# Optimization experiments

Hardware: AMD Instinct MI355X
Metric: run time of the kernel (lower is better)

The kernel has to match this reference:

```python
import jax, jax.numpy as jnp
import numpy as np

N_NODES = 50000
N_EDGES = 800000
IN_FEATS = 32
OUT_FEATS = 32
NUM_HEADS = 4


def setup_inputs() -> dict:
    key = jax.random.key(0)
    ks = jax.random.split(key, 12)
    H, F, IN = NUM_HEADS, OUT_FEATS, IN_FEATS
    h = jax.random.normal(ks[0], (N_NODES, IN), dtype=jnp.float32)
    src = jax.random.randint(ks[1], (N_EDGES,), 0, N_NODES, dtype=jnp.int64)
    dst = jax.random.randint(ks[2], (N_EDGES,), 0, N_NODES, dtype=jnp.int64)
    s = 0.1
    W_gat = jax.random.normal(ks[3], (IN, H * F), dtype=jnp.float32) * s
    attn_l = jax.random.normal(ks[4], (H, F), dtype=jnp.float32) * s
    attn_r = jax.random.normal(ks[5], (H, F), dtype=jnp.float32) * s
    W_ih = jax.random.normal(ks[6], (3 * F, H * F), dtype=jnp.float32) * s
    W_hh = jax.random.normal(ks[7], (3 * F, F), dtype=jnp.float32) * s
    b_ih = jax.random.normal(ks[8], (3 * F,), dtype=jnp.float32) * s
    b_hh = jax.random.normal(ks[9], (3 * F,), dtype=jnp.float32) * s
    return {"h": h, "W_gat": W_gat, "attn_l": attn_l, "attn_r": attn_r,
            "W_ih": W_ih, "W_hh": W_hh, "b_ih": b_ih, "b_hh": b_hh,
            "src": src, "dst": dst}


def reference(h, W_gat, attn_l, attn_r, W_ih, W_hh, b_ih, b_hh, src, dst):
    N = h.shape[0]
    H, F = attn_l.shape
    # --- GATConv ---
    feat = (h @ W_gat).reshape(N, H, F)                      # (N,H,F)
    el = jnp.einsum('nhf,hf->nh', feat, attn_l)              # (N,H)
    er = jnp.einsum('nhf,hf->nh', feat, attn_r)              # (N,H)
    e = jax.nn.leaky_relu(el[src] + er[dst], 0.2)            # (E,H) edge logits
    emax = jax.ops.segment_max(e, dst, num_segments=N)       # per-dst max (stable)
    ee = jnp.exp(e - emax[dst])
    denom = jax.ops.segment_sum(ee, dst, num_segments=N)
    alpha = ee / denom[dst]                                  # segment softmax (E,H)
    msg = feat[src] * alpha[:, :, None]                      # (E,H,F)
    agg = jax.ops.segment_sum(msg, dst, num_segments=N)      # (N,H,F)
    x = agg.reshape(N, H * F)
    # --- GRUCell (torch semantics, gate order r,z,n) ---
    gi = x @ W_ih.T + b_ih                                   # (N,3F)
    gh = h @ W_hh.T + b_hh                                   # (N,3F)
    i_r, i_z, i_n = jnp.split(gi, 3, axis=1)
    h_r, h_z, h_n = jnp.split(gh, 3, axis=1)
    r = jax.nn.sigmoid(i_r + h_r)
    z = jax.nn.sigmoid(i_z + h_z)
    n = jnp.tanh(i_n + r * h_n)
    h_new = (1.0 - z) * n + z * h
    return jax.nn.elu(h_new)
```

## Files before the change

### kernel.cpp

```cpp
#include <hip/hip_runtime.h>
#include <hip/hip_bf16.h>
#include <cmath>

#define N_NODES 50000
#define N_EDGES 800000
#define CAP 64

#define NBINS 196
#define BIN_CAP 8192
#define CUR_PAD 32

#define WCB_ITEMS (144 * 32)
#define WCB_BLOCKS (WCB_ITEMS / 256)
#define WC_ITEMS (192 * 160)
#define WC_BLOCKS (WC_ITEMS / 256)

#define P1_EPT 8
#define P1_EPB (256 * P1_EPT)
#define P1_BLOCKS ((N_EDGES + P1_EPB - 1) / P1_EPB)
#define FEAT_BLOCKS ((N_NODES / 16 + 3) / 4)

typedef __attribute__((ext_vector_type(8))) short bf16x8;
typedef __attribute__((ext_vector_type(4))) float f32x4;

__device__ inline short bfbits(float x) {
    __hip_bfloat16 t = __float2bfloat16(x);
    return *reinterpret_cast<short*>(&t);
}

__device__ inline unsigned char f32_to_fp8(float x) {
    return (unsigned char)(__builtin_amdgcn_cvt_pk_fp8_f32(x, x, 0, false) & 0xff);
}

__global__ __launch_bounds__(256) void k_prep0(
        const float* __restrict__ Wg, const float* __restrict__ al,
        const float* __restrict__ ar, const float* __restrict__ Wih,
        const float* __restrict__ Whh, __hip_bfloat16* __restrict__ Wcomb,
        __hip_bfloat16* __restrict__ Wc, int* __restrict__ bin_cursor) {
    const int t = threadIdx.x;
    if (blockIdx.x < WCB_BLOCKS) {
        const int idx = blockIdx.x * 256 + t;
        const int row = idx >> 5, k = idx & 31;
        float v = 0.f;
        if (row < 128) {
            v = Wg[k * 128 + row];
        } else if (row < 136) {
            const int hd = (row - 128) & 3;
            const float* a = (row < 132) ? (al + hd * 32) : (ar + hd * 32);
            const float* w = Wg + k * 128 + hd * 32;
#pragma unroll
            for (int f = 0; f < 32; ++f) v = fmaf(w[f], a[f], v);
        }
        Wcomb[idx] = __float2bfloat16(v);
        return;
    }
    if (blockIdx.x < WCB_BLOCKS + WC_BLOCKS) {
        const int idx = (blockIdx.x - WCB_BLOCKS) * 256 + t;
        const int r = idx / 160, k = idx - r * 160;
        float v = 0.f;
        if (r < 96) { if (k < 128) v = Wih[r * 128 + k]; }
        else        { if (k >= 128) v = Whh[(r - 96) * 32 + (k - 128)]; }
        Wc[idx] = __float2bfloat16(v);
        return;
    }
    if (t < NBINS) bin_cursor[t * CUR_PAD] = 0;
}

__global__ __launch_bounds__(256) void k_part_feat(
        const float* __restrict__ h, const __hip_bfloat16* __restrict__ Wcomb,
        const int* __restrict__ src, const int* __restrict__ dst,
        int* __restrict__ bin_cursor, unsigned* __restrict__ bin_buf,
        unsigned char* __restrict__ feat, float* __restrict__ el,
        float* __restrict__ er) {
    const int t = threadIdx.x;
    if (blockIdx.x < P1_BLOCKS) {
        __shared__ int bcnt[256], bofs[256], cur[256], gbase[256];
        __shared__ int wt4[4];
        __shared__ unsigned stage[P1_EPB];
        bcnt[t] = 0;
        __syncthreads();
        int bn[P1_EPT];
        unsigned pk[P1_EPT];
        const int ebase = blockIdx.x * P1_EPB + t * P1_EPT;
        if (ebase < N_EDGES) {
            int dd[P1_EPT], ss[P1_EPT];
            *(int4*)(dd)     = *(const int4*)(dst + ebase);
            *(int4*)(dd + 4) = *(const int4*)(dst + ebase + 4);
            *(int4*)(ss)     = *(const int4*)(src + ebase);
            *(int4*)(ss + 4) = *(const int4*)(src + ebase + 4);
#pragma unroll
            for (int q = 0; q < P1_EPT; ++q) {
                bn[q] = dd[q] >> 8;
                pk[q] = (unsigned)ss[q] | ((unsigned)(dd[q] & 255) << 16);
                atomicAdd(&bcnt[bn[q]], 1);
            }
        } else {
#pragma unroll
            for (int q = 0; q < P1_EPT; ++q) bn[q] = -1;
        }
        __syncthreads();
        {
            const int wave = t >> 6, lane = t & 63;
            const int vv = bcnt[t];
            int x = vv;
#pragma unroll
            for (int m = 1; m < 64; m <<= 1) {
                const int y = __shfl_up(x, m, 64);
                if (lane >= m) x += y;
            }
            if (lane == 63) wt4[wave] = x;
            __syncthreads();
            int wb = 0;
#pragma unroll
            for (int i = 0; i < 4; ++i) if (i < wave) wb += wt4[i];
            const int off = wb + x - vv;
            bofs[t] = off;
            cur[t] = off;
            gbase[t] = (vv > 0) ? atomicAdd(&bin_cursor[t * CUR_PAD], vv) : 0;
        }
        __syncthreads();
#pragma unroll
        for (int q = 0; q < P1_EPT; ++q)
            if (bn[q] >= 0) stage[atomicAdd(&cur[bn[q]], 1)] = pk[q];
        __syncthreads();
        if (t < NBINS) {
            const int c = bcnt[t], o = bofs[t], g = gbase[t];
            unsigned* bb = bin_buf + (size_t)t * BIN_CAP;
            for (int j = 0; j < c; ++j) {
                const int gi = g + j;
                if (gi < BIN_CAP) bb[gi] = stage[o + j];
            }
        }
        return;
    }
    __shared__ unsigned char sbuf8[4][16][136];
    const int lane = t & 63, wave = t >> 6;
    const int li = lane & 15, quad = lane >> 4;
    const int mt = (blockIdx.x - P1_BLOCKS) * 4 + wave;
    if (mt >= N_NODES / 16) return;
    const int m_base = mt * 16;
    bf16x8 a;
    {
        const float4* hp = (const float4*)(h + (size_t)(m_base + li) * 32 + quad * 8);
        const float4 f0 = hp[0], f1 = hp[1];
        a[0] = bfbits(f0.x); a[1] = bfbits(f0.y); a[2] = bfbits(f0.z); a[3] = bfbits(f0.w);
        a[4] = bfbits(f1.x); a[5] = bfbits(f1.y); a[6] = bfbits(f1.z); a[7] = bfbits(f1.w);
    }
    f32x4 acc[9];
#pragma unroll
    for (int j = 0; j < 9; ++j) acc[j] = (f32x4){0.f, 0.f, 0.f, 0.f};
#pragma unroll
    for (int j = 0; j < 9; ++j) {
        const bf16x8 b = *(const bf16x8*)(Wcomb + (size_t)(j * 16 + li) * 32 + quad * 8);
        acc[j] = __builtin_amdgcn_mfma_f32_16x16x32_bf16(a, b, acc[j], 0, 0, 0);
    }
#pragma unroll
    for (int j = 0; j < 8; ++j)
#pragma unroll
        for (int i = 0; i < 4; ++i)
            sbuf8[wave][quad * 4 + i][j * 16 + li] = f32_to_fp8(acc[j][i]);
    __builtin_amdgcn_wave_barrier();
#pragma unroll
    for (int rep = 0; rep < 4; ++rep) {
        const int row = rep * 4 + quad;
        const unsigned long long v = *(const unsigned long long*)(&sbuf8[wave][row][li * 8]);
        *(unsigned long long*)(feat + (size_t)(m_base + row) * 128 + li * 8) = v;
    }
    if (li < 8) {
#pragma unroll
        for (int i = 0; i < 4; ++i) {
            const int m = m_base + quad * 4 + i;
            if (li < 4) el[m * 4 + li] = acc[8][i];
            else        er[m * 4 + (li - 4)] = acc[8][i];
        }
    }
}

__global__ __launch_bounds__(256) void k_scat2(
        const int* __restrict__ bin_cursor, const unsigned* __restrict__ bin_buf,
        int* __restrict__ srcs_p, int* __restrict__ counts) {
    __shared__ int lcnt[256];
    const int t = threadIdx.x;
    const int b = blockIdx.x;
    lcnt[t] = 0;
    __syncthreads();
    const int cb = min(bin_cursor[b * CUR_PAD], BIN_CAP);
    const uint4* bb4 = (const uint4*)(bin_buf + (size_t)b * BIN_CAP);
    for (int i = t * 4; i < cb; i += 1024) {
        const uint4 p4 = bb4[i >> 2];
#pragma unroll
        for (int k = 0; k < 4; ++k) {
            if (i + k < cb) {
                const unsigned p = (&p4.x)[k];
                const int dl = p >> 16;
                const int s = p & 0xffff;
                const int pos = atomicAdd(&lcnt[dl], 1);
                if (pos < CAP) srcs_p[(size_t)(b * 256 + dl) * CAP + pos] = s;
            }
        }
    }
    __syncthreads();
    const int node = b * 256 + t;
    if (node < N_NODES) counts[node] = lcnt[t];
}

__global__ __launch_bounds__(256) void k_aggr_gru(
        const int* __restrict__ counts, const int* __restrict__ srcs_p,
        const unsigned char* __restrict__ feat,
        const float* __restrict__ el, const float* __restrict__ er,
        const float* __restrict__ h, const __hip_bfloat16* __restrict__ Wc,
        const float* __restrict__ bih, const float* __restrict__ bhh,
        float* __restrict__ out) {
    __shared__ __hip_bfloat16 xh_tile[16][160];
    __shared__ int   sl_s[4][4][64];
    __shared__ float ex[2][3][16][16];
    const int wave = threadIdx.x >> 6;
    const int lane = threadIdx.x & 63;
    const int eh = lane >> 5;
    const int fl = lane & 31;
    const int hq = fl >> 3;
    const int mbase = blockIdx.x * 16;

    int cnts[4];
#pragma unroll
    for (int u = 0; u < 4; ++u) {
        const int n = mbase + wave * 4 + u;
        cnts[u] = min(counts[n], CAP);
        if (lane < cnts[u]) sl_s[wave][u][lane] = srcs_p[(size_t)n * CAP + lane];
    }
    __builtin_amdgcn_wave_barrier();
    for (int u = 0; u < 4; ++u) {
        const int row = wave * 4 + u;
        const int n = mbase + row;
        const int cnt = cnts[u];
        const int* sl = sl_s[wave][u];
        const float ern = er[n * 4 + hq];
        float a0 = 0.f, a1 = 0.f, a2 = 0.f, a3 = 0.f, psum = 0.f;
        for (int i = 0; i < cnt; i += 16) {
            int  s[8];
            unsigned uq[8];
            float w[8];
#pragma unroll
            for (int j = 0; j < 8; ++j) {
                const int e2 = i + 2 * j + eh;
                s[j] = (e2 < cnt) ? sl[e2] : 0;
            }
#pragma unroll
            for (int j = 0; j < 8; ++j)
                uq[j] = *(const unsigned*)(feat + (size_t)s[j] * 128 + fl * 4);
#pragma unroll
            for (int j = 0; j < 8; ++j)
                w[j] = el[s[j] * 4 + hq];
#pragma unroll
            for (int j = 0; j < 8; ++j) {
                float v = w[j] + ern;
                v = v > 0.f ? v : 0.2f * v;
                w[j] = (i + 2 * j + eh < cnt) ? __expf(v) : 0.f;
                psum += w[j];
            }
#pragma unroll
            for (int j = 0; j < 8; ++j) {
                a0 = fmaf(w[j], __builtin_amdgcn_cvt_f32_fp8(uq[j], 0), a0);
                a1 = fmaf(w[j], __builtin_amdgcn_cvt_f32_fp8(uq[j], 1), a1);
                a2 = fmaf(w[j], __builtin_amdgcn_cvt_f32_fp8(uq[j], 2), a2);
                a3 = fmaf(w[j], __builtin_amdgcn_cvt_f32_fp8(uq[j], 3), a3);
            }
        }
        a0 += __shfl_xor(a0, 32, 64);
        a1 += __shfl_xor(a1, 32, 64);
        a2 += __shfl_xor(a2, 32, 64);
        a3 += __shfl_xor(a3, 32, 64);
        psum += __shfl_xor(psum, 1, 64);
        psum += __shfl_xor(psum, 2, 64);
        psum += __shfl_xor(psum, 4, 64);
        psum += __shfl_xor(psum, 32, 64);
        const float inv = (cnt > 0) ? 8.f / psum : 0.f;
        if (lane < 32) {
            __hip_bfloat162 p0, p1;
            p0.x = __float2bfloat16(a0 * inv); p0.y = __float2bfloat16(a1 * inv);
            p1.x = __float2bfloat16(a2 * inv); p1.y = __float2bfloat16(a3 * inv);
            __hip_bfloat162* xp = (__hip_bfloat162*)&xh_tile[row][0];
            xp[lane * 2]     = p0;
            xp[lane * 2 + 1] = p1;
            xh_tile[row][128 + lane] = __float2bfloat16(h[(size_t)n * 32 + lane]);
        }
    }
    __syncthreads();

    const int li = lane & 15, quad = lane >> 4;
    const int cb = wave >> 1;
    const int ghrole = wave & 1;
    bf16x8 a[5];
#pragma unroll
    for (int s = 0; s < 5; ++s)
        a[s] = *(const bf16x8*)((const char*)&xh_tile[0][0] + li * 320 + s * 64 + quad * 16);
    f32x4 acc[3];
#pragma unroll
    for (int g = 0; g < 3; ++g) {
        acc[g] = (f32x4){0.f, 0.f, 0.f, 0.f};
        const int j = g * 2 + cb + ghrole * 6;
        const bf16x8* bp = (const bf16x8*)(Wc + (size_t)(j * 16 + li) * 160 + quad * 8);
        acc[g] = __builtin_amdgcn_mfma_f32_16x16x32_bf16(a[0], bp[0],  acc[g], 0, 0, 0);
        acc[g] = __builtin_amdgcn_mfma_f32_16x16x32_bf16(a[1], bp[4],  acc[g], 0, 0, 0);
        acc[g] = __builtin_amdgcn_mfma_f32_16x16x32_bf16(a[2], bp[8],  acc[g], 0, 0, 0);
        acc[g] = __builtin_amdgcn_mfma_f32_16x16x32_bf16(a[3], bp[12], acc[g], 0, 0, 0);
        acc[g] = __builtin_amdgcn_mfma_f32_16x16x32_bf16(a[4], bp[16], acc[g], 0, 0, 0);
    }
    if (ghrole) {
#pragma unroll
        for (int g = 0; g < 3; ++g)
#pragma unroll
            for (int i = 0; i < 4; ++i)
                ex[cb][g][quad * 4 + i][li] = acc[g][i];
    }
    __syncthreads();
    if (!ghrole) {
        const int c = cb * 16 + li;
        const float bir = bih[c],      bhr = bhh[c];
        const float biz = bih[32 + c], bhz = bhh[32 + c];
        const float bin = bih[64 + c], bhn = bhh[64 + c];
#pragma unroll
        for (int i = 0; i < 4; ++i) {
            const int row = quad * 4 + i;
            const int m = mbase + row;
            const float gr = acc[0][i] + bir + ex[cb][0][row][li] + bhr;
            const float gz = acc[1][i] + biz + ex[cb][1][row][li] + bhz;
            const float r = 1.f / (1.f + expf(-gr));
            const float z = 1.f / (1.f + expf(-gz));
            const float nn = tanhf(acc[2][i] + bin + r * (ex[cb][2][row][li] + bhn));
            const float hv = h[(size_t)m * 32 + c];
            const float hn = (1.f - z) * nn + z * hv;
            out[(size_t)m * 32 + c] = hn > 0.f ? hn : expm1f(hn);
        }
    }
}

extern "C" void kernel_launch(void* const* d_in, const int* in_sizes, int n_in,
                              void* d_out, int out_size, void* d_ws, size_t ws_size,
                              hipStream_t stream) {
    const float* h   = (const float*)d_in[0];
    const float* Wg  = (const float*)d_in[1];
    const float* al  = (const float*)d_in[2];
    const float* ar  = (const float*)d_in[3];
    const float* Wih = (const float*)d_in[4];
    const float* Whh = (const float*)d_in[5];
    const float* bih = (const float*)d_in[6];
    const float* bhh = (const float*)d_in[7];
    const int* src   = (const int*)d_in[8];
    const int* dst   = (const int*)d_in[9];
    float* out = (float*)d_out;

    float* el = (float*)d_ws;
    float* er = el + (size_t)N_NODES * 4;
    unsigned char* feat8 = (unsigned char*)(er + (size_t)N_NODES * 4);
    __hip_bfloat16* Wc    = (__hip_bfloat16*)(feat8 + (size_t)N_NODES * 128);
    __hip_bfloat16* Wcomb = Wc + 192 * 160;
    int* counts  = (int*)(Wcomb + WCB_ITEMS);
    int* srcs_p  = counts + N_NODES;
    int* bin_cursor = srcs_p + (size_t)N_NODES * CAP;
    unsigned* bin_buf = (unsigned*)(bin_cursor + NBINS * CUR_PAD);

    k_prep0<<<WCB_BLOCKS + WC_BLOCKS + 1, 256, 0, stream>>>(
        Wg, al, ar, Wih, Whh, Wcomb, Wc, bin_cursor);
    k_part_feat<<<P1_BLOCKS + FEAT_BLOCKS, 256, 0, stream>>>(
        h, Wcomb, src, dst, bin_cursor, bin_buf, feat8, el, er);
    k_scat2<<<NBINS, 256, 0, stream>>>(bin_cursor, bin_buf, srcs_p, counts);
    k_aggr_gru<<<N_NODES / 16, 256, 0, stream>>>(
        counts, srcs_p, feat8, el, er, h, Wc, bih, bhh, out);
}
```

Baseline: 151.5 us.

## Assign one wave per destination node and share edge weights via LDS

The aggregation+GRU kernel now launches 1024-thread blocks with 16 waves, one wave per destination node, instead of 4 waves each looping over 4 nodes. Each lane computes one (edge, head) softmax weight once and shares it through LDS rather than every lane recomputing exp for its head. This is meant to raise parallelism and latency hiding for the gather and to remove redundant el loads and exponentials. In exchange, only 4 of the 16 waves run the MFMA GRU stage, the rest sit idle at the barrier, and the tighter register budget from launch bounds (1024, 8) risks spills.

```diff
diff --git a/kernel.cpp b/kernel.cpp
--- a/kernel.cpp
+++ b/kernel.cpp
@@ -204,7 +204,7 @@
     if (node < N_NODES) counts[node] = lcnt[t];
 }
 
-__global__ __launch_bounds__(256) void k_aggr_gru(
+__global__ __launch_bounds__(1024, 8) void k_aggr_gru(
         const int* __restrict__ counts, const int* __restrict__ srcs_p,
         const unsigned char* __restrict__ feat,
         const float* __restrict__ el, const float* __restrict__ er,
@@ -212,7 +212,8 @@
         const float* __restrict__ bih, const float* __restrict__ bhh,
         float* __restrict__ out) {
     __shared__ __hip_bfloat16 xh_tile[16][160];
-    __shared__ int   sl_s[4][4][64];
+    __shared__ int   sl_s[16][64];
+    __shared__ float eel_s[16][64];
     __shared__ float ex[2][3][16][16];
     const int wave = threadIdx.x >> 6;
     const int lane = threadIdx.x & 63;
@@ -220,118 +221,113 @@
     const int fl = lane & 31;
     const int hq = fl >> 3;
     const int mbase = blockIdx.x * 16;
-
-    int cnts[4];
-#pragma unroll
-    for (int u = 0; u < 4; ++u) {
-        const int n = mbase + wave * 4 + u;
-        cnts[u] = min(counts[n], CAP);
-        if (lane < cnts[u]) sl_s[wave][u][lane] = srcs_p[(size_t)n * CAP + lane];
-    }
+    const int n = mbase + wave;
+    int* sl = sl_s[wave];
+    float* eel = eel_s[wave];
+
+    const int cnt = min(counts[n], CAP);
+    sl[lane] = srcs_p[(size_t)n * CAP + lane];
+    const float ern = er[n * 4 + (lane & 3)];
     __builtin_amdgcn_wave_barrier();
-    for (int u = 0; u < 4; ++u) {
-        const int row = wave * 4 + u;
-        const int n = mbase + row;
-        const int cnt = cnts[u];
-        const int* sl = sl_s[wave][u];
-        const float ern = er[n * 4 + hq];
-        float a0 = 0.f, a1 = 0.f, a2 = 0.f, a3 = 0.f, psum = 0.f;
-        for (int i = 0; i < cnt; i += 16) {
-            int  s[8];
-            unsigned uq[8];
-            float w[8];
-#pragma unroll
-            for (int j = 0; j < 8; ++j) {
-                const int e2 = i + 2 * j + eh;
-                s[j] = (e2 < cnt) ? sl[e2] : 0;
-            }
-#pragma unroll
-            for (int j = 0; j < 8; ++j)
-                uq[j] = *(const unsigned*)(feat + (size_t)s[j] * 128 + fl * 4);
-#pragma unroll
-            for (int j = 0; j < 8; ++j)
-                w[j] = el[s[j] * 4 + hq];
-#pragma unroll
-            for (int j = 0; j < 8; ++j) {
-                float v = w[j] + ern;
-                v = v > 0.f ? v : 0.2f * v;
-                w[j] = (i + 2 * j + eh < cnt) ? __expf(v) : 0.f;
-                psum += w[j];
-            }
-#pragma unroll
-            for (int j = 0; j < 8; ++j) {
-                a0 = fmaf(w[j], __builtin_amdgcn_cvt_f32_fp8(uq[j], 0), a0);
-                a1 = fmaf(w[j], __builtin_amdgcn_cvt_f32_fp8(uq[j], 1), a1);
-                a2 = fmaf(w[j], __builtin_amdgcn_cvt_f32_fp8(uq[j], 2), a2);
-                a3 = fmaf(w[j], __builtin_amdgcn_cvt_f32_fp8(uq[j], 3), a3);
-            }
-        }
-        a0 += __shfl_xor(a0, 32, 64);
-        a1 += __shfl_xor(a1, 32, 64);
-        a2 += __shfl_xor(a2, 32, 64);
-        a3 += __shfl_xor(a3, 32, 64);
-        psum += __shfl_xor(psum, 1, 64);
-        psum += __shfl_xor(psum, 2, 64);
-        psum += __shfl_xor(psum, 4, 64);
-        psum += __shfl_xor(psum, 32, 64);
-        const float inv = (cnt > 0) ? 8.f / psum : 0.f;
-        if (lane < 32) {
-            __hip_bfloat162 p0, p1;
-            p0.x = __float2bfloat16(a0 * inv); p0.y = __float2bfloat16(a1 * inv);
-            p1.x = __float2bfloat16(a2 * inv); p1.y = __float2bfloat16(a3 * inv);
-            __hip_bfloat162* xp = (__hip_bfloat162*)&xh_tile[row][0];
-            xp[lane * 2]     = p0;
-            xp[lane * 2 + 1] = p1;
-            xh_tile[row][128 + lane] = __float2bfloat16(h[(size_t)n * 32 + lane]);
-        }
+
+    float a0 = 0.f, a1 = 0.f, a2 = 0.f, a3 = 0.f, psum = 0.f;
+    for (int i = 0; i < cnt; i += 16) {
+        int sj[8];
+#pragma unroll
+        for (int j = 0; j < 8; ++j) {
+            const int e2 = i + 2 * j + eh;
+            sj[j] = sl[e2 < cnt ? e2 : 0];
+        }
+        unsigned uq[8];
+#pragma unroll
+        for (int j = 0; j < 8; ++j)
+            uq[j] = *(const unsigned*)(feat + (size_t)sj[j] * 128 + fl * 4);
+        const int eedge = i + (lane >> 2);
+        const int sle = sl[eedge < cnt ? eedge : 0];
+        float v = el[sle * 4 + (lane & 3)] + ern;
+        v = v > 0.f ? v : 0.2f * v;
+        const float wl = (eedge < cnt) ? __expf(v) : 0.f;
+        psum += wl;
+        eel[lane] = wl;
+        __builtin_amdgcn_wave_barrier();
+#pragma unroll
+        for (int j = 0; j < 8; ++j) {
+            const float w = eel[((2 * j + eh) << 2) | hq];
+            a0 = fmaf(w, __builtin_amdgcn_cvt_f32_fp8(uq[j], 0), a0);
+            a1 = fmaf(w, __builtin_amdgcn_cvt_f32_fp8(uq[j], 1), a1);
+            a2 = fmaf(w, __builtin_amdgcn_cvt_f32_fp8(uq[j], 2), a2);
+            a3 = fmaf(w, __builtin_amdgcn_cvt_f32_fp8(uq[j], 3), a3);
+        }
+        __builtin_amdgcn_wave_barrier();
+    }
+    a0 += __shfl_xor(a0, 32, 64);
+    a1 += __shfl_xor(a1, 32, 64);
+    a2 += __shfl_xor(a2, 32, 64);
+    a3 += __shfl_xor(a3, 32, 64);
+#pragma unroll
+    for (int m = 4; m < 64; m <<= 1) psum += __shfl_xor(psum, m, 64);
+    const float dn = __shfl(psum, hq, 64);
+    const float inv = (cnt > 0) ? 1.f / dn : 0.f;
+    if (lane < 32) {
+        __hip_bfloat162 p0, p1;
+        p0.x = __float2bfloat16(a0 * inv); p0.y = __float2bfloat16(a1 * inv);
+        p1.x = __float2bfloat16(a2 * inv); p1.y = __float2bfloat16(a3 * inv);
+        __hip_bfloat162* xp = (__hip_bfloat162*)&xh_tile[wave][0];
+        xp[lane * 2]     = p0;
+        xp[lane * 2 + 1] = p1;
+        xh_tile[wave][128 + lane] = __float2bfloat16(h[(size_t)n * 32 + lane]);
     }
     __syncthreads();
 
-    const int li = lane & 15, quad = lane >> 4;
-    const int cb = wave >> 1;
-    const int ghrole = wave & 1;
-    bf16x8 a[5];
-#pragma unroll
-    for (int s = 0; s < 5; ++s)
-        a[s] = *(const bf16x8*)((const char*)&xh_tile[0][0] + li * 320 + s * 64 + quad * 16);
-    f32x4 acc[3];
-#pragma unroll
-    for (int g = 0; g < 3; ++g) {
-        acc[g] = (f32x4){0.f, 0.f, 0.f, 0.f};
-        const int j = g * 2 + cb + ghrole * 6;
-        const bf16x8* bp = (const bf16x8*)(Wc + (size_t)(j * 16 + li) * 160 + quad * 8);
-        acc[g] = __builtin_amdgcn_mfma_f32_16x16x32_bf16(a[0], bp[0],  acc[g], 0, 0, 0);
-        acc[g] = __builtin_amdgcn_mfma_f32_16x16x32_bf16(a[1], bp[4],  acc[g], 0, 0, 0);
-        acc[g] = __builtin_amdgcn_mfma_f32_16x16x32_bf16(a[2], bp[8],  acc[g], 0, 0, 0);
-        acc[g] = __builtin_amdgcn_mfma_f32_16x16x32_bf16(a[3], bp[12], acc[g], 0, 0, 0);
-        acc[g] = __builtin_amdgcn_mfma_f32_16x16x32_bf16(a[4], bp[16], acc[g], 0, 0, 0);
-    }
-    if (ghrole) {
-#pragma unroll
-        for (int g = 0; g < 3; ++g)
-#pragma unroll
-            for (int i = 0; i < 4; ++i)
-                ex[cb][g][quad * 4 + i][li] = acc[g][i];
-    }
-    __syncthreads();
-    if (!ghrole) {
-        const int c = cb * 16 + li;
-        const float bir = bih[c],      bhr = bhh[c];
-        const float biz = bih[32 + c], bhz = bhh[32 + c];
-        const float bin = bih[64 + c], bhn = bhh[64 + c];
-#pragma unroll
-        for (int i = 0; i < 4; ++i) {
-            const int row = quad * 4 + i;
-            const int m = mbase + row;
-            const float gr = acc[0][i] + bir + ex[cb][0][row][li] + bhr;
-            const float gz = acc[1][i] + biz + ex[cb][1][row][li] + bhz;
-            const float r = 1.f / (1.f + expf(-gr));
-            const float z = 1.f / (1.f + expf(-gz));
-            const float nn = tanhf(acc[2][i] + bin + r * (ex[cb][2][row][li] + bhn));
-            const float hv = h[(size_t)m * 32 + c];
-            const float hn = (1.f - z) * nn + z * hv;
-            out[(size_t)m * 32 + c] = hn > 0.f ? hn : expm1f(hn);
-        }
+    if (wave < 4) {
+        const int li = lane & 15, quad = lane >> 4;
+        const int cb = wave >> 1;
+        const int ghrole = wave & 1;
+        bf16x8 a[5];
+#pragma unroll
+        for (int s = 0; s < 5; ++s)
+            a[s] = *(const bf16x8*)((const char*)&xh_tile[0][0] + li * 320 + s * 64 + quad * 16);
+        f32x4 acc[3];
+#pragma unroll
+        for (int g = 0; g < 3; ++g) {
+            acc[g] = (f32x4){0.f, 0.f, 0.f, 0.f};
+            const int j = g * 2 + cb + ghrole * 6;
+            const bf16x8* bp = (const bf16x8*)(Wc + (size_t)(j * 16 + li) * 160 + quad * 8);
+            acc[g] = __builtin_amdgcn_mfma_f32_16x16x32_bf16(a[0], bp[0],  acc[g], 0, 0, 0);
+            acc[g] = __builtin_amdgcn_mfma_f32_16x16x32_bf16(a[1], bp[4],  acc[g], 0, 0, 0);
+            acc[g] = __builtin_amdgcn_mfma_f32_16x16x32_bf16(a[2], bp[8],  acc[g], 0, 0, 0);
+            acc[g] = __builtin_amdgcn_mfma_f32_16x16x32_bf16(a[3], bp[12], acc[g], 0, 0, 0);
+            acc[g] = __builtin_amdgcn_mfma_f32_16x16x32_bf16(a[4], bp[16], acc[g], 0, 0, 0);
+        }
+        if (ghrole) {
+#pragma unroll
+            for (int g = 0; g < 3; ++g)
+#pragma unroll
+                for (int i = 0; i < 4; ++i)
+                    ex[cb][g][quad * 4 + i][li] = acc[g][i];
+        }
+        __syncthreads();
+        if (!ghrole) {
+            const int c = cb * 16 + li;
+            const float bir = bih[c],      bhr = bhh[c];
+            const float biz = bih[32 + c], bhz = bhh[32 + c];
+            const float bin = bih[64 + c], bhn = bhh[64 + c];
+#pragma unroll
+            for (int i = 0; i < 4; ++i) {
+                const int row = quad * 4 + i;
+                const int m = mbase + row;
+                const float gr = acc[0][i] + bir + ex[cb][0][row][li] + bhr;
+                const float gz = acc[1][i] + biz + ex[cb][1][row][li] + bhz;
+                const float r = 1.f / (1.f + expf(-gr));
+                const float z = 1.f / (1.f + expf(-gz));
+                const float nn = tanhf(acc[2][i] + bin + r * (ex[cb][2][row][li] + bhn));
+                const float hv = h[(size_t)m * 32 + c];
+                const float hn = (1.f - z) * nn + z * hv;
+                out[(size_t)m * 32 + c] = hn > 0.f ? hn : expm1f(hn);
+            }
+        }
+    } else {
+        __syncthreads();
     }
 }
 
@@ -365,6 +361,6 @@
     k_part_feat<<<P1_BLOCKS + FEAT_BLOCKS, 256, 0, stream>>>(
         h, Wcomb, src, dst, bin_cursor, bin_buf, feat8, el, er);
     k_scat2<<<NBINS, 256, 0, stream>>>(bin_cursor, bin_buf, srcs_p, counts);
-    k_aggr_gru<<<N_NODES / 16, 256, 0, stream>>>(
+    k_aggr_gru<<<N_NODES / 16, 1024, 0, stream>>>(
         counts, srcs_p, feat8, el, er, h, Wc, bih, bhh, out);
 }
```

Measured after the change: 153.7 us. About the same (+1.5%).
